# Kernel tuning notes

Measured on AMD Instinct MI355X. Metric: run time of the kernel, lower is better.

## Reference

```python
import jax, jax.numpy as jnp
import numpy as np
import math

B, L, D, K, G = 4, 4096, 2048, 4, 8  # batch, seq_len, d_model, kernel_size, num_group


def setup_inputs() -> dict:
    key = jax.random.key(0)
    k1, k2 = jax.random.split(key)
    x = jax.random.normal(k1, (B, L, D), dtype=jnp.float32)
    # torch Conv1d weight is [O=D, I=D//G, K]; kaiming-uniform-ish scale.
    fan_in = (D // G) * K
    w = jax.random.normal(k2, (K, D // G, D), dtype=jnp.float32) * (1.0 / math.sqrt(fan_in))
    return {"x": x, "w": w}


def reference(x, w):
    # x: [B, L, D] (module transposes to NCL internally; we stay channels-last).
    # torch pads both sides by K-1 then slices off the trailing K-1 outputs,
    # which is exactly a left-only (causal) pad of K-1.
    k = w.shape[0]
    groups = x.shape[-1] // w.shape[1]
    out = jax.lax.conv_general_dilated(
        x, w,
        window_strides=(1,),
        padding=[(k - 1, 0)],
        dimension_numbers=("NHC", "HIO", "NHC"),
        feature_group_count=groups,
    )
    return out  # [B, L, D]
```

## Files before the change

### kernel.cpp

```cpp
#include <hip/hip_runtime.h>
#include <stdint.h>


#define CC_L 4096
#define CC_D 2048

typedef float f32x4 __attribute__((ext_vector_type(4)));
typedef __bf16 bf16x8 __attribute__((ext_vector_type(8)));

static __device__ __forceinline__ unsigned short f2bf(float f) {
    union { float f; uint32_t u; } v; v.f = f;
    uint32_t u = v.u;
    u += 0x7fffu + ((u >> 16) & 1u);
    return (unsigned short)(u >> 16);
}

static __device__ __forceinline__ void glds16(const void* g, void* l) {
    __builtin_amdgcn_global_load_lds(
        (const __attribute__((address_space(1))) uint32_t*)g,
        (__attribute__((address_space(3))) uint32_t*)l, 16, 0, 0);
}

__global__ __launch_bounds__(256) void cc_prep_w(const float* __restrict__ w,
                                                 unsigned short* __restrict__ wt) {
    __shared__ unsigned short T[64][136];
    const int tid = threadIdx.x;
    const int k  = blockIdx.x >> 6;
    const int ot = (blockIdx.x >> 1) & 31;
    const int ih = blockIdx.x & 1;
    const int o0 = ot << 6;
    const int i0 = ih << 7;

#pragma unroll
    for (int it = 0; it < 8; ++it) {
        int i  = it * 16 + (tid >> 4);
        int oc = (tid & 15) << 2;
        const float4 v = *(const float4*)(w + ((size_t)(k * 256 + i0 + i)) * CC_D + o0 + oc);
        T[oc + 0][i] = f2bf(v.x);
        T[oc + 1][i] = f2bf(v.y);
        T[oc + 2][i] = f2bf(v.z);
        T[oc + 3][i] = f2bf(v.w);
    }
    __syncthreads();
#pragma unroll
    for (int it = 0; it < 4; ++it) {
        int o  = it * 16 + (tid >> 4);
        int ic = (tid & 15) << 3;
        *(uint4*)(wt + (size_t)(o0 + o) * 1024 + k * 256 + i0 + ic) = *(const uint4*)&T[o][ic];
    }
}

__global__ __launch_bounds__(256, 3) void cc_conv(const float* __restrict__ x,
                                                  const unsigned short* __restrict__ wt,
                                                  float* __restrict__ out) {
    __shared__ unsigned short As[131][72];
    __shared__ unsigned short Bs[2][128][64];

    const int tid   = threadIdx.x;
    const int tileN = blockIdx.x & 15;
    const int tileM = blockIdx.x >> 4;
    const int n0    = tileN << 7;
    const int g     = tileN >> 1;
    const int cin   = g << 8;
    const int m0    = tileM << 7;
    const int b     = m0 >> 12;
    const int l0    = m0 & (CC_L - 1);

    const int lane = tid & 63;
    const int wv   = tid >> 6;
    const int wm   = (wv & 1) << 6;
    const int wn   = (wv >> 1) << 6;
    const int lr   = lane & 15;
    const int quad = lane >> 4;

    const int b_row = lane >> 3;
    const int b_q   = (lane & 7) ^ b_row;

    const float* xg = x + (size_t)b * CC_L * CC_D + cin;

    f32x4 acc[4][4];
#pragma unroll
    for (int i = 0; i < 4; ++i)
#pragma unroll
        for (int j = 0; j < 4; ++j) acc[i][j] = (f32x4){0.f, 0.f, 0.f, 0.f};

    const int f4 = tid & 15;
    const int rb = tid >> 4;
    float4 avm[8];
    float4 avh;

#define LOAD_A(cc)                                                                  \
    {                                                                               \
        _Pragma("unroll")                                                           \
        for (int j = 0; j < 8; ++j) {                                               \
            int l = l0 + rb + j * 16;                                               \
            avm[j] = *(const float4*)(xg + (size_t)l * CC_D + ((cc) << 6) + (f4 << 2)); \
        }                                                                           \
        if (tid < 48) {                                                             \
            int l = l0 - 3 + (tid >> 4);                                            \
            avh = *(const float4*)(xg + (size_t)(l < 0 ? 0 : l) * CC_D + ((cc) << 6) + (f4 << 2)); \
        }                                                                           \
    }

#define WRITE_A()                                                                   \
    {                                                                               \
        _Pragma("unroll")                                                           \
        for (int j = 0; j < 8; ++j) {                                               \
            ushort4 h;                                                              \
            h.x = f2bf(avm[j].x); h.y = f2bf(avm[j].y);                             \
            h.z = f2bf(avm[j].z); h.w = f2bf(avm[j].w);                             \
            *(ushort4*)&As[rb + j * 16 + 3][f4 << 2] = h;                           \
        }                                                                           \
        if (tid < 48) {                                                             \
            ushort4 h = {0, 0, 0, 0};                                               \
            if (l0 > 0) {                                                           \
                h.x = f2bf(avh.x); h.y = f2bf(avh.y);                               \
                h.z = f2bf(avh.z); h.w = f2bf(avh.w);                               \
            }                                                                       \
            *(ushort4*)&As[tid >> 4][f4 << 2] = h;                                  \
        }                                                                           \
    }

#define ISSUE_B(buf, stp)                                                           \
    {                                                                               \
        const unsigned short* gb = wt + (size_t)n0 * 1024 + (((stp) & 3) << 8)      \
                                   + (((stp) >> 2) << 6);                           \
        _Pragma("unroll")                                                           \
        for (int it = 0; it < 4; ++it) {                                            \
            int rowbase = (wv << 5) + (it << 3);                                    \
            glds16(gb + (size_t)(rowbase + b_row) * 1024 + (b_q << 3),              \
                   &Bs[buf][rowbase][0]);                                           \
        }                                                                           \
    }

    LOAD_A(0);
    ISSUE_B(0, 0);
    WRITE_A();
    LOAD_A(1);
    __syncthreads();

    for (int s = 0; s < 16; ++s) {
        if (s < 15) ISSUE_B((s + 1) & 1, s + 1);
        const int kf = s & 3;
        const int pb = s & 1;
#pragma unroll
        for (int ks = 0; ks < 2; ++ks) {
            bf16x8 a[4], bb[4];
#pragma unroll
            for (int f = 0; f < 4; ++f)
                a[f] = *(const bf16x8*)&As[wm + f * 16 + lr + kf][(ks << 5) + (quad << 3)];
#pragma unroll
            for (int f = 0; f < 4; ++f) {
                int n    = wn + f * 16 + lr;
                int slot = ((ks << 2) + quad) ^ (lr & 7);
                bb[f] = *(const bf16x8*)&Bs[pb][n][slot << 3];
            }
#pragma unroll
            for (int fm = 0; fm < 4; ++fm)
#pragma unroll
                for (int fn = 0; fn < 4; ++fn)
                    acc[fm][fn] = __builtin_amdgcn_mfma_f32_16x16x32_bf16(
                        a[fm], bb[fn], acc[fm][fn], 0, 0, 0);
        }
        if (kf == 3 && s < 15) {
            __syncthreads();
            WRITE_A();
            int ccn = (s >> 2) + 2;
            if (ccn < 4) LOAD_A(ccn);
        }
        if (s < 15) __syncthreads();
    }

    const size_t obase = (size_t)m0 * CC_D + n0;
#pragma unroll
    for (int fm = 0; fm < 4; ++fm)
#pragma unroll
        for (int fn = 0; fn < 4; ++fn) {
            int ml = wm + fm * 16 + quad * 4;
            int nl = wn + fn * 16 + lr;
#pragma unroll
            for (int r = 0; r < 4; ++r)
                out[obase + (size_t)(ml + r) * CC_D + nl] = acc[fm][fn][r];
        }
}

extern "C" void kernel_launch(void* const* d_in, const int* in_sizes, int n_in,
                              void* d_out, int out_size, void* d_ws, size_t ws_size,
                              hipStream_t stream) {
    const float* x = (const float*)d_in[0];
    const float* w = (const float*)d_in[1];
    float* out = (float*)d_out;
    unsigned short* wt = (unsigned short*)d_ws;

    cc_prep_w<<<256, 256, 0, stream>>>(w, wt);
    cc_conv<<<2048, 256, 0, stream>>>(x, wt, out);
}
```

Before: 264.2 us.

## Enlarge conv tile to 256x256 with 512 threads and double-buffered A/B pipeline

Each block now computes a 256x256 output tile (a full group) with 8 waves instead of 128x128 with 4 waves. The A tile (x rows plus causal halo) is double-buffered in swizzled LDS, and the weight layout is permuted so each k-step covers one 64-channel chunk across all taps. Global loads, LDS writes and MFMA phases are interleaved with explicit barriers, waitcnts and setprio. The aim is to halve redundant x reads and conversions and hide latency. In exchange it uses far more LDS and registers (acc[8][4]), leaving only 512 blocks.

```diff
diff --git a/kernel.cpp b/kernel.cpp
--- a/kernel.cpp
+++ b/kernel.cpp
@@ -13,6 +13,10 @@
     uint32_t u = v.u;
     u += 0x7fffu + ((u >> 16) & 1u);
     return (unsigned short)(u >> 16);
+}
+
+static __device__ __forceinline__ uint32_t pk2(float a, float b) {
+    return (uint32_t)f2bf(a) | ((uint32_t)f2bf(b) << 16);
 }
 
 static __device__ __forceinline__ void glds16(const void* g, void* l) {
@@ -46,142 +50,225 @@
     for (int it = 0; it < 4; ++it) {
         int o  = it * 16 + (tid >> 4);
         int ic = (tid & 15) << 3;
-        *(uint4*)(wt + (size_t)(o0 + o) * 1024 + k * 256 + i0 + ic) = *(const uint4*)&T[o][ic];
-    }
-}
-
-__global__ __launch_bounds__(256, 3) void cc_conv(const float* __restrict__ x,
+        int ch = i0 + ic;
+        int kk = ((ch >> 6) << 8) + (k << 6) + (ch & 63);
+        *(uint4*)(wt + (size_t)(o0 + o) * 1024 + kk) = *(const uint4*)&T[o][ic];
+    }
+}
+
+#define A_BYTES 33280
+#define B_BYTES 32768
+#define LDSA(buf) ((buf) * A_BYTES)
+#define LDSB(buf) (2 * A_BYTES + (buf) * B_BYTES)
+
+#define ISSUE_B4(bbuf, ss) {                                                    \
+    const unsigned short* gsrc_ = wg + (ss) * 64 + (b_q << 3);                  \
+    _Pragma("unroll")                                                           \
+    for (int j_ = 0; j_ < 4; ++j_) {                                            \
+        const int rowb_ = (wv << 5) + (j_ << 3);                                \
+        glds16(gsrc_ + (size_t)(rowb_ + b_sub) * 1024,                          \
+               (void*)&lds[LDSB(bbuf) + (rowb_ << 7)]);                         \
+    }                                                                           \
+}
+
+#define LOAD_A_SLOT(kk, cbn) {                                                  \
+    const int r_  = (kk) * 64 + a_r;                                            \
+    const int xr_ = l0 - 3 + r_;                                                \
+    const float* p_ = xg + (size_t)xr_ * CC_D + ((cbn) << 6) + (a_c8 << 3);     \
+    av[kk][0] = (f32x4){0.f, 0.f, 0.f, 0.f};                                    \
+    av[kk][1] = (f32x4){0.f, 0.f, 0.f, 0.f};                                    \
+    if (xr_ >= 0) { av[kk][0] = *(const f32x4*)p_;                              \
+                    av[kk][1] = *(const f32x4*)(p_ + 4); }                      \
+}
+
+#define LOAD_A_EXTRA(cbn) {                                                     \
+    if (tid < 24) {                                                             \
+        const int xr_ = l0 + 253 + (tid >> 3);                                  \
+        const float* p_ = xg + (size_t)xr_ * CC_D + ((cbn) << 6) + (a_c8 << 3); \
+        ah[0] = *(const f32x4*)p_;                                              \
+        ah[1] = *(const f32x4*)(p_ + 4);                                        \
+    }                                                                           \
+}
+
+#define WRITE_A_SLOT(kk, dbuf) {                                                \
+    const int r_ = (kk) * 64 + a_r;                                             \
+    uint4 hv_;                                                                  \
+    hv_.x = pk2(av[kk][0][0], av[kk][0][1]);                                    \
+    hv_.y = pk2(av[kk][0][2], av[kk][0][3]);                                    \
+    hv_.z = pk2(av[kk][1][0], av[kk][1][1]);                                    \
+    hv_.w = pk2(av[kk][1][2], av[kk][1][3]);                                    \
+    *(uint4*)&lds[LDSA(dbuf) + r_ * 128 + a_sw16] = hv_;                        \
+}
+
+#define WRITE_A_EXTRA(dbuf) {                                                   \
+    if (tid < 24) {                                                             \
+        const int r_ = 256 + (tid >> 3);                                        \
+        uint4 hv_;                                                              \
+        hv_.x = pk2(ah[0][0], ah[0][1]);                                        \
+        hv_.y = pk2(ah[0][2], ah[0][3]);                                        \
+        hv_.z = pk2(ah[1][0], ah[1][1]);                                        \
+        hv_.w = pk2(ah[1][2], ah[1][3]);                                        \
+        *(uint4*)&lds[LDSA(dbuf) + r_ * 128 + a_sw16] = hv_;                    \
+    }                                                                           \
+}
+
+#define ARD(dst, fm, ks, abuf) {                                                \
+    dst = *(const bf16x8*)&lds[LDSA(abuf) + (ar_row + (fm) * 16) * 128 +        \
+            (((((ks) << 2) + quad) ^ a_rsw) << 4)];                             \
+}
+#define BRD(dst, fn, ks, bbuf) {                                                \
+    dst = *(const bf16x8*)&lds[LDSB(bbuf) + (b_rowrd + (fn) * 16) * 128 +       \
+            (((((ks) << 2) + quad) ^ b_rsw) << 4)];                             \
+}
+
+#define MFMA8(fm, x0, x1) {                                                     \
+    _Pragma("unroll")                                                           \
+    for (int fn_ = 0; fn_ < 4; ++fn_) {                                         \
+        acc[fm][fn_] = __builtin_amdgcn_mfma_f32_16x16x32_bf16(                 \
+            x0, br[fn_][0], acc[fm][fn_], 0, 0, 0);                             \
+        acc[fm][fn_] = __builtin_amdgcn_mfma_f32_16x16x32_bf16(                 \
+            x1, br[fn_][1], acc[fm][fn_], 0, 0, 0);                             \
+    }                                                                           \
+}
+
+#define LGKM0() { asm volatile("s_waitcnt lgkmcnt(0)");                         \
+                  __builtin_amdgcn_sched_barrier(0); }
+#define SBAR()  __builtin_amdgcn_s_barrier()
+
+__global__ __launch_bounds__(512, 2) void cc_conv(const float* __restrict__ x,
                                                   const unsigned short* __restrict__ wt,
                                                   float* __restrict__ out) {
-    __shared__ unsigned short As[131][72];
-    __shared__ unsigned short Bs[2][128][64];
+    __shared__ __align__(16) unsigned char lds[2 * A_BYTES + 2 * B_BYTES];
 
     const int tid   = threadIdx.x;
-    const int tileN = blockIdx.x & 15;
-    const int tileM = blockIdx.x >> 4;
-    const int n0    = tileN << 7;
-    const int g     = tileN >> 1;
-    const int cin   = g << 8;
-    const int m0    = tileM << 7;
+    const int tileN = blockIdx.x & 7;
+    const int tileM = blockIdx.x >> 3;
+    const int n0    = tileN << 8;
+    const int m0    = tileM << 8;
     const int b     = m0 >> 12;
     const int l0    = m0 & (CC_L - 1);
 
     const int lane = tid & 63;
     const int wv   = tid >> 6;
-    const int wm   = (wv & 1) << 6;
+    const int wm   = (wv & 1) << 7;
     const int wn   = (wv >> 1) << 6;
     const int lr   = lane & 15;
     const int quad = lane >> 4;
 
-    const int b_row = lane >> 3;
-    const int b_q   = (lane & 7) ^ b_row;
-
-    const float* xg = x + (size_t)b * CC_L * CC_D + cin;
-
-    f32x4 acc[4][4];
-#pragma unroll
-    for (int i = 0; i < 4; ++i)
+    const int b_sub   = lane >> 3;
+    const int b_q     = (lane & 7) ^ b_sub;
+    const int b_rowrd = wn + lr;
+    const int b_rsw   = lr & 7;
+
+    const int a_r    = tid >> 3;
+    const int a_c8   = tid & 7;
+    const int a_sw16 = (a_c8 ^ (a_r & 7)) << 4;
+
+    const float* xg = x + (size_t)b * CC_L * CC_D + n0;
+    const unsigned short* wg = wt + (size_t)n0 * 1024;
+
+    f32x4 acc[8][4];
+#pragma unroll
+    for (int i = 0; i < 8; ++i)
 #pragma unroll
         for (int j = 0; j < 4; ++j) acc[i][j] = (f32x4){0.f, 0.f, 0.f, 0.f};
 
-    const int f4 = tid & 15;
-    const int rb = tid >> 4;
-    float4 avm[8];
-    float4 avh;
-
-#define LOAD_A(cc)                                                                  \
-    {                                                                               \
-        _Pragma("unroll")                                                           \
-        for (int j = 0; j < 8; ++j) {                                               \
-            int l = l0 + rb + j * 16;                                               \
-            avm[j] = *(const float4*)(xg + (size_t)l * CC_D + ((cc) << 6) + (f4 << 2)); \
-        }                                                                           \
-        if (tid < 48) {                                                             \
-            int l = l0 - 3 + (tid >> 4);                                            \
-            avh = *(const float4*)(xg + (size_t)(l < 0 ? 0 : l) * CC_D + ((cc) << 6) + (f4 << 2)); \
-        }                                                                           \
-    }
-
-#define WRITE_A()                                                                   \
-    {                                                                               \
-        _Pragma("unroll")                                                           \
-        for (int j = 0; j < 8; ++j) {                                               \
-            ushort4 h;                                                              \
-            h.x = f2bf(avm[j].x); h.y = f2bf(avm[j].y);                             \
-            h.z = f2bf(avm[j].z); h.w = f2bf(avm[j].w);                             \
-            *(ushort4*)&As[rb + j * 16 + 3][f4 << 2] = h;                           \
-        }                                                                           \
-        if (tid < 48) {                                                             \
-            ushort4 h = {0, 0, 0, 0};                                               \
-            if (l0 > 0) {                                                           \
-                h.x = f2bf(avh.x); h.y = f2bf(avh.y);                               \
-                h.z = f2bf(avh.z); h.w = f2bf(avh.w);                               \
-            }                                                                       \
-            *(ushort4*)&As[tid >> 4][f4 << 2] = h;                                  \
-        }                                                                           \
-    }
-
-#define ISSUE_B(buf, stp)                                                           \
-    {                                                                               \
-        const unsigned short* gb = wt + (size_t)n0 * 1024 + (((stp) & 3) << 8)      \
-                                   + (((stp) >> 2) << 6);                           \
-        _Pragma("unroll")                                                           \
-        for (int it = 0; it < 4; ++it) {                                            \
-            int rowbase = (wv << 5) + (it << 3);                                    \
-            glds16(gb + (size_t)(rowbase + b_row) * 1024 + (b_q << 3),              \
-                   &Bs[buf][rowbase][0]);                                           \
-        }                                                                           \
-    }
-
-    LOAD_A(0);
-    ISSUE_B(0, 0);
-    WRITE_A();
-    LOAD_A(1);
-    __syncthreads();
-
-    for (int s = 0; s < 16; ++s) {
-        if (s < 15) ISSUE_B((s + 1) & 1, s + 1);
-        const int kf = s & 3;
-        const int pb = s & 1;
-#pragma unroll
-        for (int ks = 0; ks < 2; ++ks) {
-            bf16x8 a[4], bb[4];
-#pragma unroll
-            for (int f = 0; f < 4; ++f)
-                a[f] = *(const bf16x8*)&As[wm + f * 16 + lr + kf][(ks << 5) + (quad << 3)];
-#pragma unroll
-            for (int f = 0; f < 4; ++f) {
-                int n    = wn + f * 16 + lr;
-                int slot = ((ks << 2) + quad) ^ (lr & 7);
-                bb[f] = *(const bf16x8*)&Bs[pb][n][slot << 3];
-            }
-#pragma unroll
-            for (int fm = 0; fm < 4; ++fm)
-#pragma unroll
-                for (int fn = 0; fn < 4; ++fn)
-                    acc[fm][fn] = __builtin_amdgcn_mfma_f32_16x16x32_bf16(
-                        a[fm], bb[fn], acc[fm][fn], 0, 0, 0);
+    f32x4 av[4][2];
+    f32x4 ah[2];
+
+#pragma unroll
+    for (int k = 0; k < 4; ++k) LOAD_A_SLOT(k, 0);
+    LOAD_A_EXTRA(0);
+    ISSUE_B4(0, 0);
+    __builtin_amdgcn_sched_barrier(0);
+#pragma unroll
+    for (int k = 0; k < 4; ++k) WRITE_A_SLOT(k, 0);
+    WRITE_A_EXTRA(0);
+    asm volatile("s_waitcnt vmcnt(0) lgkmcnt(0)" ::: "memory");
+    __builtin_amdgcn_sched_barrier(0);
+    SBAR();
+
+#pragma unroll
+    for (int cb = 0; cb < 4; ++cb) {
+#pragma unroll
+        for (int t = 0; t < 4; ++t) {
+            const int s   = cb * 4 + t;
+            const int ab  = cb & 1;
+            const int bb_ = t & 1;
+            const int ar_row = wm + lr + t;
+            const int a_rsw  = (lr + t) & 7;
+            bf16x8 br[4][2];
+            bf16x8 aq[4][2];
+
+            if (s < 15) ISSUE_B4(bb_ ^ 1, s + 1);
+            __builtin_amdgcn_sched_barrier(0);
+            if (t == 0 && cb < 3) LOAD_A_EXTRA(cb + 1);
+#pragma unroll
+            for (int fn = 0; fn < 4; ++fn) {
+                BRD(br[fn][0], fn, 0, bb_);
+                BRD(br[fn][1], fn, 1, bb_);
+            }
+#pragma unroll
+            for (int fm = 0; fm < 4; ++fm) {
+                ARD(aq[fm][0], fm, 0, ab);
+                ARD(aq[fm][1], fm, 1, ab);
+            }
+            SBAR();
+            LGKM0();
+            __builtin_amdgcn_s_setprio(1);
+            MFMA8(0, aq[0][0], aq[0][1]);
+            MFMA8(1, aq[1][0], aq[1][1]);
+            MFMA8(2, aq[2][0], aq[2][1]);
+            MFMA8(3, aq[3][0], aq[3][1]);
+            __builtin_amdgcn_s_setprio(0);
+            SBAR();
+
+            if (t < 2) { if (cb < 3) LOAD_A_SLOT(2 * t + 0, cb + 1); }
+            else       { if (cb < 3) WRITE_A_SLOT(2 * (t - 2) + 0, ab ^ 1); }
+            ARD(aq[0][0], 4, 0, ab); ARD(aq[0][1], 4, 1, ab);
+            ARD(aq[1][0], 5, 0, ab); ARD(aq[1][1], 5, 1, ab);
+            SBAR();
+            LGKM0();
+            __builtin_amdgcn_s_setprio(1);
+            MFMA8(4, aq[0][0], aq[0][1]);
+            MFMA8(5, aq[1][0], aq[1][1]);
+            __builtin_amdgcn_s_setprio(0);
+            SBAR();
+
+            if (t < 2) { if (cb < 3) LOAD_A_SLOT(2 * t + 1, cb + 1); }
+            else if (cb < 3) {
+                WRITE_A_SLOT(2 * (t - 2) + 1, ab ^ 1);
+                if (t == 3) WRITE_A_EXTRA(ab ^ 1);
+            }
+            ARD(aq[0][0], 6, 0, ab); ARD(aq[0][1], 6, 1, ab);
+            ARD(aq[1][0], 7, 0, ab); ARD(aq[1][1], 7, 1, ab);
+            SBAR();
+            LGKM0();
+            __builtin_amdgcn_s_setprio(1);
+            MFMA8(6, aq[0][0], aq[0][1]);
+            MFMA8(7, aq[1][0], aq[1][1]);
+            __builtin_amdgcn_s_setprio(0);
+            if (s < 15) {
+                if (t < 2 && cb < 3) { asm volatile("s_waitcnt vmcnt(4)" ::: "memory"); }
+                else                 { asm volatile("s_waitcnt vmcnt(0)" ::: "memory"); }
+                __builtin_amdgcn_sched_barrier(0);
+            }
+            SBAR();
         }
-        if (kf == 3 && s < 15) {
-            __syncthreads();
-            WRITE_A();
-            int ccn = (s >> 2) + 2;
-            if (ccn < 4) LOAD_A(ccn);
-        }
-        if (s < 15) __syncthreads();
     }
 
     const size_t obase = (size_t)m0 * CC_D + n0;
 #pragma unroll
-    for (int fm = 0; fm < 4; ++fm)
+    for (int fm = 0; fm < 8; ++fm) {
+        const int ml = wm + fm * 16 + (quad << 2);
 #pragma unroll
         for (int fn = 0; fn < 4; ++fn) {
-            int ml = wm + fm * 16 + quad * 4;
-            int nl = wn + fn * 16 + lr;
+            const int nl = wn + fn * 16 + lr;
 #pragma unroll
             for (int r = 0; r < 4; ++r)
                 out[obase + (size_t)(ml + r) * CC_D + nl] = acc[fm][fn][r];
         }
+    }
 }
 
 extern "C" void kernel_launch(void* const* d_in, const int* in_sizes, int n_in,
@@ -193,5 +280,5 @@
     unsigned short* wt = (unsigned short*)d_ws;
 
     cc_prep_w<<<256, 256, 0, stream>>>(w, wt);
-    cc_conv<<<2048, 256, 0, stream>>>(x, wt, out);
-}
+    cc_conv<<<512, 512, 0, stream>>>(x, wt, out);
+}
```

Result: slower. 330.5 us (+25.1%).
